# Performance work log

Measured on AMD Instinct MI355X. Metric: run time of the kernel, lower is better.

The kernel has to match this reference:

```python
import jax, jax.numpy as jnp
import numpy as np

IN_DIM = 512
OUT_DIM = 512
DEGREE = 3
KNOTS = (0.2, 0.4, 0.6, 0.8)
SDIM = DEGREE + 1 + len(KNOTS)  # 8
BATCH = 2048


def truncated_power_basis(t):
    # t: (B,) -> (B, SDIM)
    cols = [jnp.ones_like(t)]
    for p in range(1, DEGREE + 1):
        cols.append(t ** p)
    for c in KNOTS:  # degree > 1 branch: relu(t - knot)^degree
        cols.append(jax.nn.relu(t - c) ** DEGREE)
    return jnp.stack(cols, axis=1)


def setup_inputs() -> dict:
    key = jax.random.key(0)
    k0, k1, k2 = jax.random.split(key, 3)
    inputs = jax.random.uniform(k0, (BATCH, IN_DIM + 1), dtype=jnp.float32)
    # xavier_uniform for W_wts (fan_in=SDIM, fan_out=IN_DIM*OUT_DIM)
    limW = float(np.sqrt(6.0 / (SDIM + IN_DIM * OUT_DIM)))
    W_wts = jax.random.uniform(k1, (SDIM, IN_DIM * OUT_DIM), dtype=jnp.float32,
                               minval=-limW, maxval=limW)
    limb = float(np.sqrt(6.0 / (SDIM + OUT_DIM)))
    b_wts = jax.random.uniform(k2, (SDIM, OUT_DIM), dtype=jnp.float32,
                               minval=-limb, maxval=limb)
    return {"inputs": inputs, "W_wts": W_wts, "b_wts": b_wts}


def reference(inputs, W_wts, b_wts):
    treatment = inputs[:, 0]          # (B,)
    features = inputs[:, 1:]          # (B, IN_DIM)
    basis = truncated_power_basis(treatment)  # (B, SDIM)
    Wk = W_wts.reshape(SDIM, IN_DIM, OUT_DIM)
    # fused: per-sample weight W[b] = sum_s basis[b,s] * Wk[s]; out[b] = features[b] @ W[b]
    out = jnp.einsum('bs,bi,sio->bo', basis, features, Wk)
    out = out + basis @ b_wts         # (B, OUT_DIM)
    return out
```

## Files before the change

### kernel.cpp

```cpp
#include <hip/hip_runtime.h>
#include <stdint.h>

#define BATCH   2048
#define INDIM   512
#define OUTDIM  512
#define SDIM    8
#define KTOT    4096
#define SPLITK  4

typedef __attribute__((ext_vector_type(4))) float  f32x4;
typedef __attribute__((ext_vector_type(8))) __bf16 bf16x8;
typedef __attribute__((ext_vector_type(8))) unsigned short u16x8;

__device__ __forceinline__ unsigned short f2bf(float x) {
  unsigned int u = __float_as_uint(x);
  u += 0x7fffu + ((u >> 16) & 1u);
  return (unsigned short)(u >> 16);
}

__device__ __forceinline__ void llds16(const void* g, void* s) {
  __builtin_amdgcn_global_load_lds(
      (__attribute__((address_space(1))) void*)g,
      (__attribute__((address_space(3))) void*)s, 16, 0, 0);
}

__device__ __forceinline__ void mkbasis(float t, float* bs) {
  bs[0] = 1.0f; bs[1] = t; bs[2] = t * t; bs[3] = bs[2] * t;
  const float kn[4] = {0.2f, 0.4f, 0.6f, 0.8f};
#pragma unroll
  for (int c = 0; c < 4; ++c) {
    float d = fmaxf(t - kn[c], 0.0f);
    bs[4 + c] = d * d * d;
  }
}

__global__ __launch_bounds__(256) void prep_kernel(
    const float* __restrict__ inp, const float* __restrict__ W,
    const float* __restrict__ bwts, unsigned short* __restrict__ Fbf,
    unsigned short* __restrict__ Btf, float* __restrict__ Bas,
    float* __restrict__ out) {
  const int tid = threadIdx.x;
  const int bx  = blockIdx.x;
  if (bx < 512) {
    const int kt = bx >> 3, ntile = bx & 7;
    const int k0 = kt * 64, n0 = ntile * 64;
    __shared__ float Ts[64][65];
#pragma unroll
    for (int p = 0; p < 4; ++p) {
      const int r  = (tid >> 4) + p * 16;
      const int c4 = (tid & 15) * 4;
      float4 v = *(const float4*)&W[(size_t)(k0 + r) * 512 + n0 + c4];
      Ts[c4 + 0][r] = v.x; Ts[c4 + 1][r] = v.y;
      Ts[c4 + 2][r] = v.z; Ts[c4 + 3][r] = v.w;
    }
    __syncthreads();
    const int nl  = tid >> 2;
    const int kcc = (tid & 3) * 16;
    u16x8 o0, o1;
#pragma unroll
    for (int q = 0; q < 8; ++q) {
      o0[q] = f2bf(Ts[nl][kcc + q]);
      o1[q] = f2bf(Ts[nl][kcc + 8 + q]);
    }
    unsigned short* dst = Btf + (size_t)(n0 + nl) * KTOT + k0 + kcc;
    *(u16x8*)dst = o0;
    *(u16x8*)(dst + 8) = o1;
  } else if (bx < 1024) {
    const int b0   = (bx - 512) * 4;
    const int b    = b0 + (tid >> 6);
    const int i0   = (tid & 63) * 8;
    const float* row = inp + (size_t)b * (INDIM + 1);
    u16x8 o;
#pragma unroll
    for (int q = 0; q < 8; ++q) o[q] = f2bf(row[1 + i0 + q]);
    *(u16x8*)(Fbf + (size_t)b * INDIM + i0) = o;
    if (tid < 4) {
      const int bb = b0 + tid;
      float t = inp[(size_t)bb * (INDIM + 1)];
      float bs[8]; mkbasis(t, bs);
      f32x4 lo = {bs[0], bs[1], bs[2], bs[3]};
      f32x4 hi = {bs[4], bs[5], bs[6], bs[7]};
      *(f32x4*)(Bas + (size_t)bb * 8)     = lo;
      *(f32x4*)(Bas + (size_t)bb * 8 + 4) = hi;
    }
  } else {
    const int bb = (bx - 1024) * 2 + (tid >> 7);
    const int o0 = (tid & 127) * 4;
    float t = inp[(size_t)bb * (INDIM + 1)];
    float bs[8]; mkbasis(t, bs);
    float4 a = make_float4(0.f, 0.f, 0.f, 0.f);
#pragma unroll
    for (int s = 0; s < 8; ++s) {
      float4 wv = *(const float4*)&bwts[s * OUTDIM + o0];
      a.x += bs[s] * wv.x; a.y += bs[s] * wv.y;
      a.z += bs[s] * wv.z; a.w += bs[s] * wv.w;
    }
    *(float4*)&out[(size_t)bb * OUTDIM + o0] = a;
  }
}

__global__ __launch_bounds__(256, 4) void gemm_kernel(
    const unsigned short* __restrict__ Fbf,
    const unsigned short* __restrict__ Btf,
    const float* __restrict__ Bas,
    float* __restrict__ out) {
  const int tid  = threadIdx.x;
  const int kc   = blockIdx.x & (SPLITK - 1);
  const int tile = blockIdx.x >> 2;
  const int nt = tile & 7, mt = tile >> 3;
  const int m0 = mt * 64, n0 = nt * 64;
  const int l = tid & 63, w = tid >> 6;
  const int wm = w >> 1, wn = w & 1;
  const int quad = l >> 4, lr = l & 15;

  __shared__ __align__(16) unsigned short As[64 * 64];
  __shared__ __align__(16) unsigned short Bs[64 * 64];

  f32x4 m00 = {}, m01 = {}, m10 = {}, m11 = {};

  const int sr = tid >> 3, pc = tid & 7;
  const int lc = pc ^ (sr & 7);
  const unsigned short* Ag = Fbf + (size_t)(m0 + sr) * INDIM + lc * 8;
  const unsigned short* Bg = Btf + (size_t)(n0 + sr) * KTOT + lc * 8;
  unsigned short* AsW = &As[sr * 64 + pc * 8];
  unsigned short* BsW = &Bs[sr * 64 + pc * 8];

  const int sx  = lr & 7;
  const int ar  = (wm * 32 + lr) * 64;
  const int br  = (wn * 32 + lr) * 64;
  const int c0  = ((0 + quad) ^ sx) * 8;
  const int c1  = ((4 + quad) ^ sx) * 8;

  const float* bp = Bas + (size_t)(m0 + wm * 32 + quad * 4) * 8;

#pragma unroll
  for (int sl = 0; sl < 2; ++sl) {
    const int s = kc * 2 + sl;
    const unsigned short* Bk = Bg + (size_t)s * 512;
    f32x4 p00 = {}, p01 = {}, p10 = {}, p11 = {};
    for (int ib = 0; ib < 8; ++ib) {
      const int ka = ib * 64;
      llds16(Ag + ka,               AsW);
      llds16(Ag + ka + 32 * INDIM,  AsW + 32 * 64);
      llds16(Bk + ka,               BsW);
      llds16(Bk + ka + 32 * KTOT,   BsW + 32 * 64);
      __syncthreads();

      bf16x8 a00 = *(const bf16x8*)&As[ar + c0];
      bf16x8 a10 = *(const bf16x8*)&As[ar + 1024 + c0];
      bf16x8 b00 = *(const bf16x8*)&Bs[br + c0];
      bf16x8 b10 = *(const bf16x8*)&Bs[br + 1024 + c0];
      bf16x8 a01 = *(const bf16x8*)&As[ar + c1];
      bf16x8 a11 = *(const bf16x8*)&As[ar + 1024 + c1];
      bf16x8 b01 = *(const bf16x8*)&Bs[br + c1];
      bf16x8 b11 = *(const bf16x8*)&Bs[br + 1024 + c1];

      p00 = __builtin_amdgcn_mfma_f32_16x16x32_bf16(a00, b00, p00, 0, 0, 0);
      p01 = __builtin_amdgcn_mfma_f32_16x16x32_bf16(a00, b10, p01, 0, 0, 0);
      p10 = __builtin_amdgcn_mfma_f32_16x16x32_bf16(a10, b00, p10, 0, 0, 0);
      p11 = __builtin_amdgcn_mfma_f32_16x16x32_bf16(a10, b10, p11, 0, 0, 0);
      p00 = __builtin_amdgcn_mfma_f32_16x16x32_bf16(a01, b01, p00, 0, 0, 0);
      p01 = __builtin_amdgcn_mfma_f32_16x16x32_bf16(a01, b11, p01, 0, 0, 0);
      p10 = __builtin_amdgcn_mfma_f32_16x16x32_bf16(a11, b01, p10, 0, 0, 0);
      p11 = __builtin_amdgcn_mfma_f32_16x16x32_bf16(a11, b11, p11, 0, 0, 0);

      __syncthreads();
    }
#pragma unroll
    for (int r = 0; r < 4; ++r) {
      const float f0 = bp[r * 8 + s];
      const float f1 = bp[(16 + r) * 8 + s];
      m00[r] += p00[r] * f0; m01[r] += p01[r] * f0;
      m10[r] += p10[r] * f1; m11[r] += p11[r] * f1;
    }
  }

  const int col = n0 + wn * 32 + lr;
  const int row = m0 + wm * 32 + quad * 4;
  float* o00 = out + (size_t)row * OUTDIM + col;
#pragma unroll
  for (int r = 0; r < 4; ++r) {
    unsafeAtomicAdd(o00 + (size_t)r * OUTDIM,             m00[r]);
    unsafeAtomicAdd(o00 + (size_t)r * OUTDIM + 16,        m01[r]);
    unsafeAtomicAdd(o00 + (size_t)(16 + r) * OUTDIM,      m10[r]);
    unsafeAtomicAdd(o00 + (size_t)(16 + r) * OUTDIM + 16, m11[r]);
  }
}

extern "C" void kernel_launch(void* const* d_in, const int* in_sizes, int n_in,
                              void* d_out, int out_size, void* d_ws, size_t ws_size,
                              hipStream_t stream) {
  const float* inp  = (const float*)d_in[0];
  const float* W    = (const float*)d_in[1];
  const float* bwts = (const float*)d_in[2];
  float* out = (float*)d_out;

  unsigned short* Fbf = (unsigned short*)d_ws;
  unsigned short* Btf = Fbf + (size_t)BATCH * INDIM;
  float*          Bas = (float*)(Btf + (size_t)OUTDIM * KTOT);

  prep_kernel<<<2048, 256, 0, stream>>>(inp, W, bwts, Fbf, Btf, Bas, out);
  gemm_kernel<<<(BATCH / 64) * (OUTDIM / 64) * SPLITK, 256, 0, stream>>>(Fbf, Btf, Bas, out);
}
```

Baseline: 92.96 us.

## Drop split-K atomics, keep A tile resident in LDS, double-buffer B

Removes the 4-way split over spline terms, so each block computes a full 64x64 output tile across all 8 basis terms and writes it directly with the bias added, instead of using atomic adds. The 64x512 feature tile is loaded into LDS once (64 KB) and reused for all 8 terms, while B tiles are double-buffered so the next load overlaps the current MFMAs. The cost is 4x fewer blocks (256 on a large GPU), lower occupancy from the 72 KB of LDS, and an extra bias buffer round trip through workspace.

```diff
diff --git a/kernel.cpp b/kernel.cpp
--- a/kernel.cpp
+++ b/kernel.cpp
@@ -6,7 +6,6 @@
 #define OUTDIM  512
 #define SDIM    8
 #define KTOT    4096
-#define SPLITK  4
 
 typedef __attribute__((ext_vector_type(4))) float  f32x4;
 typedef __attribute__((ext_vector_type(8))) __bf16 bf16x8;
@@ -38,7 +37,7 @@
     const float* __restrict__ inp, const float* __restrict__ W,
     const float* __restrict__ bwts, unsigned short* __restrict__ Fbf,
     unsigned short* __restrict__ Btf, float* __restrict__ Bas,
-    float* __restrict__ out) {
+    float* __restrict__ BiasP) {
   const int tid = threadIdx.x;
   const int bx  = blockIdx.x;
   if (bx < 512) {
@@ -95,65 +94,79 @@
       a.x += bs[s] * wv.x; a.y += bs[s] * wv.y;
       a.z += bs[s] * wv.z; a.w += bs[s] * wv.w;
     }
-    *(float4*)&out[(size_t)bb * OUTDIM + o0] = a;
-  }
-}
-
-__global__ __launch_bounds__(256, 4) void gemm_kernel(
+    *(float4*)&BiasP[(size_t)bb * OUTDIM + o0] = a;
+  }
+}
+
+__global__ __launch_bounds__(256, 2) void gemm_kernel(
     const unsigned short* __restrict__ Fbf,
     const unsigned short* __restrict__ Btf,
     const float* __restrict__ Bas,
+    const float* __restrict__ BiasP,
     float* __restrict__ out) {
   const int tid  = threadIdx.x;
-  const int kc   = blockIdx.x & (SPLITK - 1);
-  const int tile = blockIdx.x >> 2;
+  const int tile = blockIdx.x;
   const int nt = tile & 7, mt = tile >> 3;
   const int m0 = mt * 64, n0 = nt * 64;
   const int l = tid & 63, w = tid >> 6;
   const int wm = w >> 1, wn = w & 1;
   const int quad = l >> 4, lr = l & 15;
 
-  __shared__ __align__(16) unsigned short As[64 * 64];
-  __shared__ __align__(16) unsigned short Bs[64 * 64];
+  __shared__ __align__(16) unsigned short Af[64 * 512];
+  __shared__ __align__(16) unsigned short Bs[2][64 * 64];
 
   f32x4 m00 = {}, m01 = {}, m10 = {}, m11 = {};
+
+  {
+    const int rsub = tid >> 6;
+    const int pc64 = tid & 63;
+#pragma unroll
+    for (int rd = 0; rd < 16; ++rd) {
+      const int row  = rd * 4 + rsub;
+      const int lc64 = pc64 ^ (row & 7);
+      llds16(Fbf + (size_t)(m0 + row) * INDIM + lc64 * 8,
+             &Af[(size_t)rd * 2048 + tid * 8]);
+    }
+  }
 
   const int sr = tid >> 3, pc = tid & 7;
   const int lc = pc ^ (sr & 7);
-  const unsigned short* Ag = Fbf + (size_t)(m0 + sr) * INDIM + lc * 8;
   const unsigned short* Bg = Btf + (size_t)(n0 + sr) * KTOT + lc * 8;
-  unsigned short* AsW = &As[sr * 64 + pc * 8];
-  unsigned short* BsW = &Bs[sr * 64 + pc * 8];
 
   const int sx  = lr & 7;
-  const int ar  = (wm * 32 + lr) * 64;
+  const int arA = (wm * 32 + lr) * 512;
   const int br  = (wn * 32 + lr) * 64;
-  const int c0  = ((0 + quad) ^ sx) * 8;
-  const int c1  = ((4 + quad) ^ sx) * 8;
+  const int cB0 = ((0 + quad) ^ sx) * 8;
+  const int cB1 = ((4 + quad) ^ sx) * 8;
+
+  llds16(Bg,              &Bs[0][tid * 8]);
+  llds16(Bg + 32 * KTOT,  &Bs[0][tid * 8 + 32 * 64]);
+  __syncthreads();
 
   const float* bp = Bas + (size_t)(m0 + wm * 32 + quad * 4) * 8;
 
-#pragma unroll
-  for (int sl = 0; sl < 2; ++sl) {
-    const int s = kc * 2 + sl;
-    const unsigned short* Bk = Bg + (size_t)s * 512;
+  for (int s = 0; s < 8; ++s) {
     f32x4 p00 = {}, p01 = {}, p10 = {}, p11 = {};
+#pragma unroll
     for (int ib = 0; ib < 8; ++ib) {
-      const int ka = ib * 64;
-      llds16(Ag + ka,               AsW);
-      llds16(Ag + ka + 32 * INDIM,  AsW + 32 * 64);
-      llds16(Bk + ka,               BsW);
-      llds16(Bk + ka + 32 * KTOT,   BsW + 32 * 64);
-      __syncthreads();
-
-      bf16x8 a00 = *(const bf16x8*)&As[ar + c0];
-      bf16x8 a10 = *(const bf16x8*)&As[ar + 1024 + c0];
-      bf16x8 b00 = *(const bf16x8*)&Bs[br + c0];
-      bf16x8 b10 = *(const bf16x8*)&Bs[br + 1024 + c0];
-      bf16x8 a01 = *(const bf16x8*)&As[ar + c1];
-      bf16x8 a11 = *(const bf16x8*)&As[ar + 1024 + c1];
-      bf16x8 b01 = *(const bf16x8*)&Bs[br + c1];
-      bf16x8 b11 = *(const bf16x8*)&Bs[br + 1024 + c1];
+      const int t   = s * 8 + ib;
+      const int cur = t & 1;
+      if (t < 63) {
+        const unsigned short* Bn = Bg + (size_t)(t + 1) * 64;
+        llds16(Bn,             &Bs[cur ^ 1][tid * 8]);
+        llds16(Bn + 32 * KTOT, &Bs[cur ^ 1][tid * 8 + 32 * 64]);
+      }
+      const int cA0 = ib * 64 + ((0 + quad) ^ sx) * 8;
+      const int cA1 = ib * 64 + ((4 + quad) ^ sx) * 8;
+
+      bf16x8 a00 = *(const bf16x8*)&Af[arA + cA0];
+      bf16x8 a10 = *(const bf16x8*)&Af[arA + 16 * 512 + cA0];
+      bf16x8 a01 = *(const bf16x8*)&Af[arA + cA1];
+      bf16x8 a11 = *(const bf16x8*)&Af[arA + 16 * 512 + cA1];
+      bf16x8 b00 = *(const bf16x8*)&Bs[cur][br + cB0];
+      bf16x8 b10 = *(const bf16x8*)&Bs[cur][br + 1024 + cB0];
+      bf16x8 b01 = *(const bf16x8*)&Bs[cur][br + cB1];
+      bf16x8 b11 = *(const bf16x8*)&Bs[cur][br + 1024 + cB1];
 
       p00 = __builtin_amdgcn_mfma_f32_16x16x32_bf16(a00, b00, p00, 0, 0, 0);
       p01 = __builtin_amdgcn_mfma_f32_16x16x32_bf16(a00, b10, p01, 0, 0, 0);
@@ -177,13 +190,14 @@
 
   const int col = n0 + wn * 32 + lr;
   const int row = m0 + wm * 32 + quad * 4;
-  float* o00 = out + (size_t)row * OUTDIM + col;
+  const float* bsrc = BiasP + (size_t)row * OUTDIM + col;
+  float* o = out + (size_t)row * OUTDIM + col;
 #pragma unroll
   for (int r = 0; r < 4; ++r) {
-    unsafeAtomicAdd(o00 + (size_t)r * OUTDIM,             m00[r]);
-    unsafeAtomicAdd(o00 + (size_t)r * OUTDIM + 16,        m01[r]);
-    unsafeAtomicAdd(o00 + (size_t)(16 + r) * OUTDIM,      m10[r]);
-    unsafeAtomicAdd(o00 + (size_t)(16 + r) * OUTDIM + 16, m11[r]);
+    o[(size_t)r * OUTDIM]             = m00[r] + bsrc[(size_t)r * OUTDIM];
+    o[(size_t)r * OUTDIM + 16]        = m01[r] + bsrc[(size_t)r * OUTDIM + 16];
+    o[(size_t)(16 + r) * OUTDIM]      = m10[r] + bsrc[(size_t)(16 + r) * OUTDIM];
+    o[(size_t)(16 + r) * OUTDIM + 16] = m11[r] + bsrc[(size_t)(16 + r) * OUTDIM + 16];
   }
 }
 
@@ -198,7 +212,8 @@
   unsigned short* Fbf = (unsigned short*)d_ws;
   unsigned short* Btf = Fbf + (size_t)BATCH * INDIM;
   float*          Bas = (float*)(Btf + (size_t)OUTDIM * KTOT);
-
-  prep_kernel<<<2048, 256, 0, stream>>>(inp, W, bwts, Fbf, Btf, Bas, out);
-  gemm_kernel<<<(BATCH / 64) * (OUTDIM / 64) * SPLITK, 256, 0, stream>>>(Fbf, Btf, Bas, out);
-}
+  float*          BiasP = Bas + (size_t)BATCH * SDIM;
+
+  prep_kernel<<<2048, 256, 0, stream>>>(inp, W, bwts, Fbf, Btf, Bas, BiasP);
+  gemm_kernel<<<(BATCH / 64) * (OUTDIM / 64), 256, 0, stream>>>(Fbf, Btf, Bas, BiasP, out);
+}
```

Result: slower. 102.3 us (+10.1%).

## Enlarge GEMM tiles to 128x128 and split K across all basis slices

Applied to the files above, without the earlier changes.

The block tile grows from 64x64 to 128x128, and each wave now computes a 64x64 sub-tile with a 4x4 grid of MFMA accumulators. This raises operand reuse from LDS and cuts global and LDS traffic per MFMA. Split-K goes from 4 to 8, so each block handles exactly one basis slice and applies the basis scaling once before its atomic adds. In exchange the number of float atomics into the output doubles, and the grid shrinks to 512 blocks with lower occupancy (launch bounds 2), which may leave compute units underused.

```diff
diff --git a/kernel.cpp b/kernel.cpp
--- a/kernel.cpp
+++ b/kernel.cpp
@@ -6,7 +6,7 @@
 #define OUTDIM  512
 #define SDIM    8
 #define KTOT    4096
-#define SPLITK  4
+#define SPLITK  8
 
 typedef __attribute__((ext_vector_type(4))) float  f32x4;
 typedef __attribute__((ext_vector_type(8))) __bf16 bf16x8;
@@ -99,91 +99,86 @@
   }
 }
 
-__global__ __launch_bounds__(256, 4) void gemm_kernel(
+__global__ __launch_bounds__(256, 2) void gemm_kernel(
     const unsigned short* __restrict__ Fbf,
     const unsigned short* __restrict__ Btf,
     const float* __restrict__ Bas,
     float* __restrict__ out) {
   const int tid  = threadIdx.x;
-  const int kc   = blockIdx.x & (SPLITK - 1);
-  const int tile = blockIdx.x >> 2;
-  const int nt = tile & 7, mt = tile >> 3;
-  const int m0 = mt * 64, n0 = nt * 64;
+  const int s    = blockIdx.x & (SPLITK - 1);
+  const int tile = blockIdx.x >> 3;
+  const int nt = tile & 3, mt = tile >> 2;
+  const int m0 = mt * 128, n0 = nt * 128;
   const int l = tid & 63, w = tid >> 6;
   const int wm = w >> 1, wn = w & 1;
   const int quad = l >> 4, lr = l & 15;
 
-  __shared__ __align__(16) unsigned short As[64 * 64];
-  __shared__ __align__(16) unsigned short Bs[64 * 64];
+  __shared__ __align__(16) unsigned short As[128 * 64];
+  __shared__ __align__(16) unsigned short Bs[128 * 64];
 
-  f32x4 m00 = {}, m01 = {}, m10 = {}, m11 = {};
+  f32x4 acc[4][4] = {};
 
   const int sr = tid >> 3, pc = tid & 7;
   const int lc = pc ^ (sr & 7);
   const unsigned short* Ag = Fbf + (size_t)(m0 + sr) * INDIM + lc * 8;
-  const unsigned short* Bg = Btf + (size_t)(n0 + sr) * KTOT + lc * 8;
-  unsigned short* AsW = &As[sr * 64 + pc * 8];
-  unsigned short* BsW = &Bs[sr * 64 + pc * 8];
+  const unsigned short* Bg = Btf + (size_t)(n0 + sr) * KTOT + (size_t)s * 512 + lc * 8;
 
-  const int sx  = lr & 7;
-  const int ar  = (wm * 32 + lr) * 64;
-  const int br  = (wn * 32 + lr) * 64;
-  const int c0  = ((0 + quad) ^ sx) * 8;
-  const int c1  = ((4 + quad) ^ sx) * 8;
+  const int sx = lr & 7;
+  const int c0 = (quad ^ sx) * 8;
+  const int c1 = ((4 + quad) ^ sx) * 8;
+  int arow[4], brow[4];
+#pragma unroll
+  for (int i = 0; i < 4; ++i) {
+    arow[i] = (wm * 64 + i * 16 + lr) * 64;
+    brow[i] = (wn * 64 + i * 16 + lr) * 64;
+  }
 
-  const float* bp = Bas + (size_t)(m0 + wm * 32 + quad * 4) * 8;
+  for (int it = 0; it < 8; ++it) {
+    const int koff = it * 64;
+#pragma unroll
+    for (int j = 0; j < 4; ++j) {
+      llds16(Ag + koff + (size_t)(j * 32) * INDIM, &As[j * 2048 + tid * 8]);
+      llds16(Bg + koff + (size_t)(j * 32) * KTOT,  &Bs[j * 2048 + tid * 8]);
+    }
+    __syncthreads();
 
+    bf16x8 a0[4], a1[4], b0[4], b1[4];
 #pragma unroll
-  for (int sl = 0; sl < 2; ++sl) {
-    const int s = kc * 2 + sl;
-    const unsigned short* Bk = Bg + (size_t)s * 512;
-    f32x4 p00 = {}, p01 = {}, p10 = {}, p11 = {};
-    for (int ib = 0; ib < 8; ++ib) {
-      const int ka = ib * 64;
-      llds16(Ag + ka,               AsW);
-      llds16(Ag + ka + 32 * INDIM,  AsW + 32 * 64);
-      llds16(Bk + ka,               BsW);
-      llds16(Bk + ka + 32 * KTOT,   BsW + 32 * 64);
-      __syncthreads();
-
-      bf16x8 a00 = *(const bf16x8*)&As[ar + c0];
-      bf16x8 a10 = *(const bf16x8*)&As[ar + 1024 + c0];
-      bf16x8 b00 = *(const bf16x8*)&Bs[br + c0];
-      bf16x8 b10 = *(const bf16x8*)&Bs[br + 1024 + c0];
-      bf16x8 a01 = *(const bf16x8*)&As[ar + c1];
-      bf16x8 a11 = *(const bf16x8*)&As[ar + 1024 + c1];
-      bf16x8 b01 = *(const bf16x8*)&Bs[br + c1];
-      bf16x8 b11 = *(const bf16x8*)&Bs[br + 1024 + c1];
-
-      p00 = __builtin_amdgcn_mfma_f32_16x16x32_bf16(a00, b00, p00, 0, 0, 0);
-      p01 = __builtin_amdgcn_mfma_f32_16x16x32_bf16(a00, b10, p01, 0, 0, 0);
-      p10 = __builtin_amdgcn_mfma_f32_16x16x32_bf16(a10, b00, p10, 0, 0, 0);
-      p11 = __builtin_amdgcn_mfma_f32_16x16x32_bf16(a10, b10, p11, 0, 0, 0);
-      p00 = __builtin_amdgcn_mfma_f32_16x16x32_bf16(a01, b01, p00, 0, 0, 0);
-      p01 = __builtin_amdgcn_mfma_f32_16x16x32_bf16(a01, b11, p01, 0, 0, 0);
-      p10 = __builtin_amdgcn_mfma_f32_16x16x32_bf16(a11, b01, p10, 0, 0, 0);
-      p11 = __builtin_amdgcn_mfma_f32_16x16x32_bf16(a11, b11, p11, 0, 0, 0);
-
-      __syncthreads();
+    for (int i = 0; i < 4; ++i) {
+      a0[i] = *(const bf16x8*)&As[arow[i] + c0];
+      a1[i] = *(const bf16x8*)&As[arow[i] + c1];
+      b0[i] = *(const bf16x8*)&Bs[brow[i] + c0];
+      b1[i] = *(const bf16x8*)&Bs[brow[i] + c1];
     }
 #pragma unroll
-    for (int r = 0; r < 4; ++r) {
-      const float f0 = bp[r * 8 + s];
-      const float f1 = bp[(16 + r) * 8 + s];
-      m00[r] += p00[r] * f0; m01[r] += p01[r] * f0;
-      m10[r] += p10[r] * f1; m11[r] += p11[r] * f1;
-    }
+    for (int i = 0; i < 4; ++i)
+#pragma unroll
+      for (int j = 0; j < 4; ++j) {
+        acc[i][j] = __builtin_amdgcn_mfma_f32_16x16x32_bf16(a0[i], b0[j], acc[i][j], 0, 0, 0);
+        acc[i][j] = __builtin_amdgcn_mfma_f32_16x16x32_bf16(a1[i], b1[j], acc[i][j], 0, 0, 0);
+      }
+    __syncthreads();
   }
 
-  const int col = n0 + wn * 32 + lr;
-  const int row = m0 + wm * 32 + quad * 4;
-  float* o00 = out + (size_t)row * OUTDIM + col;
+  float bsv[4][4];
 #pragma unroll
-  for (int r = 0; r < 4; ++r) {
-    unsafeAtomicAdd(o00 + (size_t)r * OUTDIM,             m00[r]);
-    unsafeAtomicAdd(o00 + (size_t)r * OUTDIM + 16,        m01[r]);
-    unsafeAtomicAdd(o00 + (size_t)(16 + r) * OUTDIM,      m10[r]);
-    unsafeAtomicAdd(o00 + (size_t)(16 + r) * OUTDIM + 16, m11[r]);
+  for (int i = 0; i < 4; ++i) {
+    const int rowb = m0 + wm * 64 + i * 16 + quad * 4;
+#pragma unroll
+    for (int r = 0; r < 4; ++r)
+      bsv[i][r] = Bas[(size_t)(rowb + r) * 8 + s];
+  }
+#pragma unroll
+  for (int i = 0; i < 4; ++i) {
+    const int rowb = m0 + wm * 64 + i * 16 + quad * 4;
+#pragma unroll
+    for (int j = 0; j < 4; ++j) {
+      const int col = n0 + wn * 64 + j * 16 + lr;
+      float* o = out + (size_t)rowb * OUTDIM + col;
+#pragma unroll
+      for (int r = 0; r < 4; ++r)
+        unsafeAtomicAdd(o + (size_t)r * OUTDIM, acc[i][j][r] * bsv[i][r]);
+    }
   }
 }
 
@@ -200,5 +195,5 @@
   float*          Bas = (float*)(Btf + (size_t)OUTDIM * KTOT);
 
   prep_kernel<<<2048, 256, 0, stream>>>(inp, W, bwts, Fbf, Btf, Bas, out);
-  gemm_kernel<<<(BATCH / 64) * (OUTDIM / 64) * SPLITK, 256, 0, stream>>>(Fbf, Btf, Bas, out);
+  gemm_kernel<<<(BATCH / 128) * (OUTDIM / 128) * SPLITK, 256, 0, stream>>>(Fbf, Btf, Bas, out);
 }
```

Result: slower. 102.4 us (+10.2%).
